# Optimization experiments

Measured on AMD Instinct MI355X. Metric: run time of the kernel, lower is better.

The kernel has to match this reference:

```python
import jax, jax.numpy as jnp
import numpy as np

B, H, W, C = 8, 128, 128, 192
G, K = 6, 3
K2 = K * K
GC = C // G
OFFSET_SCALE = 0.1
DN = ('NHWC', 'HWIO', 'NHWC')


def setup_inputs() -> dict:
    key = jax.random.key(0)
    ks = jax.random.split(key, 8)
    s = 1.0 / np.sqrt(C)
    return {
        'x': jax.random.normal(ks[0], (B, H, W, C), jnp.float32),
        'w_in': jax.random.normal(ks[1], (C, C), jnp.float32) * s,
        'b_in': jnp.zeros((C,), jnp.float32),
        'w_dw': jax.random.normal(ks[2], (3, 3, 1, C), jnp.float32) / 3.0,  # depthwise 3x3, HWIO
        'b_dw': jnp.zeros((C,), jnp.float32),
        'w_pw': jax.random.normal(ks[3], (1, 1, C, C), jnp.float32) * s,  # 1x1 conv
        'b_pw': jnp.zeros((C,), jnp.float32),
        'w_off': jax.random.normal(ks[4], (C, G * K2 * 2), jnp.float32) * 0.01,
        'b_off': jnp.zeros((G * K2 * 2,), jnp.float32),
        'w_mask': jax.random.normal(ks[5], (C, G * K2), jnp.float32) * 0.01,
        'b_mask': jnp.zeros((G * K2,), jnp.float32),
        'w_out': jax.random.normal(ks[6], (C, C), jnp.float32) * s,
        'b_out': jnp.zeros((C,), jnp.float32),
    }


def _deform_forward(x, w_in, b_in, w_dw, b_dw, w_pw, b_pw, w_off, b_off, w_mask, b_mask, w_out, b_out):
    x_proj = x @ w_in + b_in  # [B,H,W,C]

    # dw_conv: depthwise 3x3 -> SiLU -> 1x1 pointwise (all channels-last)
    xd = jax.lax.conv_general_dilated(x, w_dw, (1, 1), 'SAME', dimension_numbers=DN,
                                      feature_group_count=C) + b_dw
    xd = xd * jax.nn.sigmoid(xd)  # SiLU
    xd = jax.lax.conv_general_dilated(xd, w_pw, (1, 1), 'SAME', dimension_numbers=DN) + b_pw

    offsets = (xd @ w_off + b_off).reshape(B, H, W, G, K2, 2) * OFFSET_SCALE
    attn = jax.nn.softmax((xd @ w_mask + b_mask).reshape(B, H, W, G, K2), axis=-1)
    attn = jnp.nan_to_num(attn, nan=0.0)

    r = jnp.arange(-(K // 2), K // 2 + 1, dtype=jnp.float32)
    ref_grid = jnp.stack(jnp.meshgrid(r, r, indexing='ij'), -1).reshape(K2, 2)  # [K2,2]
    pos = ref_grid + offsets  # [B,H,W,G,K2,2]
    pos_h = jnp.clip(pos[..., 0] + jnp.arange(H, dtype=jnp.float32)[None, :, None, None, None], 0.0, H - 1)
    pos_w = jnp.clip(pos[..., 1] + jnp.arange(W, dtype=jnp.float32)[None, None, :, None, None], 0.0, W - 1)

    xg = x_proj.reshape(B, H * W, G, GC)

    def gather(hi, wi):
        idx = (hi * W + wi).reshape(B, H * W, G, 1)
        return jnp.take_along_axis(xg, idx, axis=1).reshape(B, H, W, G, GC)

    def tap(acc, inputs):
        ph, pw, a = inputs  # each [B,H,W,G]
        hf = jnp.clip(ph.astype(jnp.int32), 0, H - 1)
        wf = jnp.clip(pw.astype(jnp.int32), 0, W - 1)
        hc = jnp.minimum(hf + 1, H - 1)
        wc = jnp.minimum(wf + 1, W - 1)
        hw = ph - hf.astype(jnp.float32)
        ww = pw - wf.astype(jnp.float32)
        sampled = (gather(hf, wf) * ((1 - hw) * (1 - ww))[..., None]
                   + gather(hf, wc) * ((1 - hw) * ww)[..., None]
                   + gather(hc, wf) * (hw * (1 - ww))[..., None]
                   + gather(hc, wc) * (hw * ww)[..., None])
        return acc + sampled * a[..., None], None

    xs = (jnp.moveaxis(pos_h, -1, 0), jnp.moveaxis(pos_w, -1, 0), jnp.moveaxis(attn, -1, 0))
    out, _ = jax.lax.scan(tap, jnp.zeros((B, H, W, G, GC), x.dtype), xs)
    return out.reshape(B, H, W, C) @ w_out + b_out


def reference(x, w_in, b_in, w_dw, b_dw, w_pw, b_pw, w_off, b_off, w_mask, b_mask, w_out, b_out):
    return _deform_forward(x, w_in, b_in, w_dw, b_dw, w_pw, b_pw,
                           w_off, b_off, w_mask, b_mask, w_out, b_out)
```

## Files before the change

kernel.cpp:

```cpp
#include <hip/hip_runtime.h>
#include <hip/hip_bf16.h>

#define Bn 8
#define Hn 128
#define Wn 128
#define Cn 192
#define Gn 6
#define GCn 32
#define NPIX (Bn*Hn*Wn)

typedef __attribute__((ext_vector_type(8))) short v8s;
typedef __attribute__((ext_vector_type(4))) float v4f;
typedef __attribute__((ext_vector_type(2))) float v2f;
typedef __hip_bfloat16 bf16;

__device__ __forceinline__ float b2f(bf16 v){ return __bfloat162float(v); }
__device__ __forceinline__ float lo16(unsigned u){ return __uint_as_float(u << 16); }
__device__ __forceinline__ float hi16(unsigned u){ return __uint_as_float(u & 0xffff0000u); }
__device__ __forceinline__ v2f up2(unsigned u){
    return (v2f){ __uint_as_float(u << 16), __uint_as_float(u & 0xffff0000u) };
}

__global__ __launch_bounds__(256) void cvt_bf16(const float* __restrict__ in,
                                                bf16* __restrict__ out, long n)
{
    long base = ((long)blockIdx.x*256 + threadIdx.x)*8;
    if (base >= n) return;
    float v[8];
    *(float4*)(v)   = *(const float4*)(in + base);
    *(float4*)(v+4) = *(const float4*)(in + base + 4);
    bf16 o[8];
    #pragma unroll
    for (int j=0;j<8;j++) o[j] = __float2bfloat16(v[j]);
    *(uint4*)(out + base) = *(uint4*)o;
}

__global__ __launch_bounds__(256) void swizzle_w(const float* __restrict__ w,
                                                 bf16* __restrict__ out, int N)
{
    int idx = blockIdx.x*256 + threadIdx.x;
    int j = idx & 7, lane = (idx>>3)&63, ks = (idx>>9)%6, nt = idx/3072;
    int k = ks*32 + ((lane>>4)<<3) + j;
    int n = (nt<<4) + (lane&15);
    out[idx] = (n < N) ? __float2bfloat16(w[k*N + n]) : __float2bfloat16(0.0f);
}

__global__ __launch_bounds__(256) void swizzle_om(const float* __restrict__ woff,
        const float* __restrict__ wmask, const float* __restrict__ boff,
        const float* __restrict__ bmask, bf16* __restrict__ out, float* __restrict__ biascat)
{
    int idx = blockIdx.x*256 + threadIdx.x;
    if (idx < 192) {
        float bv = 0.0f;
        if (idx < 108) bv = boff[idx];
        else if (idx < 162) bv = bmask[idx-108];
        biascat[idx] = bv;
    }
    int j = idx & 7, lane = (idx>>3)&63, ks = (idx>>9)%6, nt = idx/3072;
    int k = ks*32 + ((lane>>4)<<3) + j;
    int n = (nt<<4) + (lane&15);
    float v = 0.0f;
    if (n < 108)      v = woff[k*108 + n];
    else if (n < 162) v = wmask[k*54 + (n-108)];
    out[idx] = __float2bfloat16(v);
}

__device__ __forceinline__ void store_out(bf16* p, float v){ *p = __float2bfloat16(v); }
__device__ __forceinline__ void store_out(float* p, float v){ *p = v; }

template<typename OutT>
__global__ __launch_bounds__(256, 2) void gemm6r(const bf16* __restrict__ A,
        const v8s* __restrict__ wfrag, const float* __restrict__ bias,
        OutT* __restrict__ Cmat, int Nreal, int Nstride)
{
    int tid = threadIdx.x;
    int wave = tid >> 6, lane = tid & 63;
    int q = lane >> 4, r = lane & 15;
    int n = blockIdx.x;
    int l = (n & 7) * 128 + (n >> 3);
    int yhalf = l & 1;
    int mt0 = l >> 1;
    const v8s* wsrc = wfrag + yhalf*(36*64) + lane;
    v8s breg[36];
    #pragma unroll
    for (int f=0; f<36; f++) breg[f] = wsrc[f*64];
    int col0 = yhalf*96;
    float bv[6];
    #pragma unroll
    for (int nt=0; nt<6; nt++) {
        int col = col0 + nt*16 + r;
        bv[nt] = (col < Nreal) ? bias[col] : 0.0f;
    }
    const int MT = NPIX/64;
    for (int mt = mt0; mt < MT; mt += 512) {
        const bf16* Ap = A + (size_t)(mt*64 + wave*16 + r)*Cn + q*8;
        v8s av[6];
        #pragma unroll
        for (int ks=0; ks<6; ks++) av[ks] = *(const v8s*)(Ap + ks*32);
        v4f acc[6];
        #pragma unroll
        for (int nt=0;nt<6;nt++) acc[nt] = (v4f){0.f,0.f,0.f,0.f};
        #pragma unroll
        for (int ks=0; ks<6; ks++)
            #pragma unroll
            for (int nt=0;nt<6;nt++)
                acc[nt] = __builtin_amdgcn_mfma_f32_16x16x32_bf16(
                              av[ks], breg[nt*6+ks], acc[nt], 0, 0, 0);
        int orow = mt*64 + wave*16 + q*4;
        #pragma unroll
        for (int nt=0;nt<6;nt++) {
            int col = col0 + nt*16 + r;
            if (col < Nreal) {
                #pragma unroll
                for (int i=0;i<4;i++)
                    store_out(&Cmat[(size_t)(orow+i)*Nstride + col], acc[nt][i] + bv[nt]);
            }
        }
    }
}

__global__ __launch_bounds__(256, 4) void dw_silu(const bf16* __restrict__ x,
        const bf16* __restrict__ wdwb, const float* __restrict__ bdw, bf16* __restrict__ out)
{
    int bid = blockIdx.x;
    int bsw = (bid & 7) * 768 + (bid >> 3);
    int idx = bsw*256 + threadIdx.x;
    int c16 = idx % 12; int pix = idx / 12;
    int b = pix >> 14; int hw = pix & 16383; int h = hw >> 7, w = hw & 127;
    int cb = c16*16;
    v2f acc2[8];
    #pragma unroll
    for (int j=0;j<8;j++) acc2[j] = (v2f){bdw[cb+2*j], bdw[cb+2*j+1]};
    #pragma unroll
    for (int dy=-1;dy<=1;dy++){
        int hh=h+dy; if ((unsigned)hh >= (unsigned)Hn) continue;
        #pragma unroll
        for (int dx=-1;dx<=1;dx++){
            int ww=w+dx; if ((unsigned)ww >= (unsigned)Wn) continue;
            const uint4* xp = (const uint4*)(x + ((size_t)((b<<14)+(hh<<7)+ww))*Cn + cb);
            const uint4* wp = (const uint4*)(wdwb + ((dy+1)*3+(dx+1))*Cn + cb);
            #pragma unroll
            for (int cs=0;cs<2;cs++){
                uint4 xu = xp[cs], wu = wp[cs];
                unsigned xa[4] = {xu.x,xu.y,xu.z,xu.w};
                unsigned wa[4] = {wu.x,wu.y,wu.z,wu.w};
                #pragma unroll
                for (int t=0;t<4;t++)
                    acc2[cs*4+t] += up2(xa[t]) * up2(wa[t]);
            }
        }
    }
    bf16 ov[16];
    #pragma unroll
    for (int j=0;j<8;j++){
        float v0 = acc2[j].x, v1 = acc2[j].y;
        ov[2*j]   = __float2bfloat16(v0 / (1.f + __expf(-v0)));
        ov[2*j+1] = __float2bfloat16(v1 / (1.f + __expf(-v1)));
    }
    uint4* op = (uint4*)(out + (size_t)pix*Cn + cb);
    op[0] = ((uint4*)ov)[0];
    op[1] = ((uint4*)ov)[1];
}


#define LOADTAP(K, S)                                                        \
  { float ph = (float)(h + (K)/3 - 1) + 0.1f*lo16(op[K]);                    \
    float pw = (float)(w + (K)%3 - 1) + 0.1f*hi16(op[K]);                    \
    ph = fminf(fmaxf(ph, 0.f), 127.f);                                       \
    pw = fminf(fmaxf(pw, 0.f), 127.f);                                       \
    int hf = (int)ph, wf = (int)pw;                                          \
    fh##S = ph - (float)hf; fw##S = pw - (float)wf;                          \
    int hc = min(hf+1,127), wc = min(wf+1,127);                              \
    const uint4* p00 = (const uint4*)(xb + ((hf<<7)+wf)*Cn);                 \
    const uint4* p01 = (const uint4*)(xb + ((hf<<7)+wc)*Cn);                 \
    const uint4* p10 = (const uint4*)(xb + ((hc<<7)+wf)*Cn);                 \
    const uint4* p11 = (const uint4*)(xb + ((hc<<7)+wc)*Cn);                 \
    S##00[0]=p00[0]; S##00[1]=p00[1]; S##01[0]=p01[0]; S##01[1]=p01[1];      \
    S##10[0]=p10[0]; S##10[1]=p10[1]; S##11[0]=p11[0]; S##11[1]=p11[1]; }

#define ACCTAP(K, S)                                                         \
  { float a = att[K];                                                        \
    float w00=(1.f-fh##S)*(1.f-fw##S)*a, w01=(1.f-fh##S)*fw##S*a,            \
          w10=fh##S*(1.f-fw##S)*a, w11=fh##S*fw##S*a;                        \
    _Pragma("unroll")                                                        \
    for (int cs=0;cs<2;cs++){                                                \
      unsigned u00[4]={S##00[cs].x,S##00[cs].y,S##00[cs].z,S##00[cs].w};     \
      unsigned u01[4]={S##01[cs].x,S##01[cs].y,S##01[cs].z,S##01[cs].w};     \
      unsigned u10[4]={S##10[cs].x,S##10[cs].y,S##10[cs].z,S##10[cs].w};     \
      unsigned u11[4]={S##11[cs].x,S##11[cs].y,S##11[cs].z,S##11[cs].w};     \
      _Pragma("unroll")                                                      \
      for (int t=0;t<4;t++)                                                  \
        acc2[cs*4+t] += up2(u00[t])*w00 + up2(u01[t])*w01                    \
                      + up2(u10[t])*w10 + up2(u11[t])*w11; } }

__global__ __launch_bounds__(256, 4) void deform_sample(const bf16* __restrict__ P,
        const bf16* __restrict__ OM, bf16* __restrict__ S)
{
    int bid = blockIdx.x;
    int bsw = (bid & 7) * 768 + (bid >> 3);
    int idx = bsw*256 + threadIdx.x;
    int half = idx & 1;
    int g = (idx >> 1) % 6;
    int pix = idx / 12;
    int b = pix >> 14; int hw = pix & 16383; int h = hw >> 7, w = hw & 127;
    const bf16* om = OM + (size_t)pix*162;
    const bf16* oml = om + 108 + g*9;
    const unsigned* ofp = (const unsigned*)(om + g*18);

    unsigned op[9];
    #pragma unroll
    for (int k=0;k<9;k++) op[k] = ofp[k];

    float att[9];
    float m = -1e30f;
    #pragma unroll
    for (int k=0;k<9;k++){ att[k] = b2f(oml[k]); m = fmaxf(m, att[k]); }
    float ssum = 0.f;
    #pragma unroll
    for (int k=0;k<9;k++){ att[k] = __expf(att[k]-m); ssum += att[k]; }
    float inv = 1.f/ssum;
    #pragma unroll
    for (int k=0;k<9;k++) att[k] *= inv;

    int chbase = g*GCn + half*16;
    const bf16* xb = P + ((((size_t)b) << 14))*Cn + chbase;

    v2f acc2[8];
    #pragma unroll
    for (int j=0;j<8;j++) acc2[j] = (v2f){0.f, 0.f};

    uint4 A00[2],A01[2],A10[2],A11[2]; float fhA,fwA;
    uint4 B00[2],B01[2],B10[2],B11[2]; float fhB,fwB;

    LOADTAP(0, A)
    LOADTAP(1, B)
    ACCTAP(0, A)  LOADTAP(2, A)
    ACCTAP(1, B)  LOADTAP(3, B)
    ACCTAP(2, A)  LOADTAP(4, A)
    ACCTAP(3, B)  LOADTAP(5, B)
    ACCTAP(4, A)  LOADTAP(6, A)
    ACCTAP(5, B)  LOADTAP(7, B)
    ACCTAP(6, A)  LOADTAP(8, A)
    ACCTAP(7, B)
    ACCTAP(8, A)

    bf16 ov[16];
    #pragma unroll
    for (int j=0;j<8;j++){
        ov[2*j]   = __float2bfloat16(acc2[j].x);
        ov[2*j+1] = __float2bfloat16(acc2[j].y);
    }
    uint4* sp = (uint4*)(S + (size_t)pix*Cn + chbase);
    sp[0] = ((uint4*)ov)[0];
    sp[1] = ((uint4*)ov)[1];
}

extern "C" void kernel_launch(void* const* d_in, const int* in_sizes, int n_in,
                              void* d_out, int out_size, void* d_ws, size_t ws_size,
                              hipStream_t stream)
{
    const float* x      = (const float*)d_in[0];
    const float* w_in   = (const float*)d_in[1];
    const float* b_in   = (const float*)d_in[2];
    const float* w_dw   = (const float*)d_in[3];
    const float* b_dw   = (const float*)d_in[4];
    const float* w_pw   = (const float*)d_in[5];
    const float* b_pw   = (const float*)d_in[6];
    const float* w_off  = (const float*)d_in[7];
    const float* b_off  = (const float*)d_in[8];
    const float* w_mask = (const float*)d_in[9];
    const float* b_mask = (const float*)d_in[10];
    const float* w_out  = (const float*)d_in[11];
    const float* b_out  = (const float*)d_in[12];
    float* out = (float*)d_out;

    char* ws = (char*)d_ws;
    size_t off = 0;
    auto carve = [&](size_t bytes)->char* {
        char* p = ws + off; off += (bytes + 255) & ~(size_t)255; return p; };
    bf16* XB  = (bf16*)carve((size_t)NPIX*Cn*2);
    bf16* P   = (bf16*)carve((size_t)NPIX*Cn*2);
    bf16* D   = (bf16*)carve((size_t)NPIX*Cn*2);
    bf16* OM  = (bf16*)carve((size_t)NPIX*162*2);
    bf16* wfI = (bf16*)carve(36864*2);
    bf16* wfP = (bf16*)carve(36864*2);
    bf16* wfO = (bf16*)carve(36864*2);
    bf16* wfM = (bf16*)carve(36864*2);
    float* bM = (float*)carve(192*4);
    bf16* WDW = (bf16*)carve(1728*2);

    dim3 blk(256);
    cvt_bf16<<<12288, blk, 0, stream>>>(x, XB, (long)NPIX*Cn);
    cvt_bf16<<<1,     blk, 0, stream>>>(w_dw, WDW, 1728);
    swizzle_w<<<144, blk, 0, stream>>>(w_in,  wfI, 192);
    swizzle_w<<<144, blk, 0, stream>>>(w_pw,  wfP, 192);
    swizzle_w<<<144, blk, 0, stream>>>(w_out, wfO, 192);
    swizzle_om<<<144, blk, 0, stream>>>(w_off, w_mask, b_off, b_mask, wfM, bM);

    gemm6r<bf16><<<1024, blk, 0, stream>>>(XB, (const v8s*)wfI, b_in, P, 192, 192);

    dw_silu<<<6144, blk, 0, stream>>>(XB, WDW, b_dw, D);

    bf16* X2 = XB;
    gemm6r<bf16><<<1024, blk, 0, stream>>>(D,  (const v8s*)wfP, b_pw, X2, 192, 192);
    gemm6r<bf16><<<1024, blk, 0, stream>>>(X2, (const v8s*)wfM, bM,  OM, 162, 162);

    deform_sample<<<6144, blk, 0, stream>>>(P, OM, D);

    gemm6r<float><<<1024, blk, 0, stream>>>(D, (const v8s*)wfO, b_out, out, 192, 192);
}
```

Before: 418.9 us.

## Fold pointwise conv weights into offset/mask projection to drop one GEMM

Because the 1x1 pointwise conv and the offset/mask projection are both linear, the two weight matrices are premultiplied (w_pw @ [w_off|w_mask]) on device, and the pw bias is folded into the combined bias. This removes a full NPIX x 192 x 192 GEMM and the intermediate X2 write and read. The combined weight is computed with a naive per-element loop of 192 MACs in the setup kernel, which adds a small cost. Rounding changes because the bf16 rounding of the intermediate is skipped.

```diff
diff --git a/kernel.cpp b/kernel.cpp
--- a/kernel.cpp
+++ b/kernel.cpp
@@ -45,24 +45,35 @@
     out[idx] = (n < N) ? __float2bfloat16(w[k*N + n]) : __float2bfloat16(0.0f);
 }
 
-__global__ __launch_bounds__(256) void swizzle_om(const float* __restrict__ woff,
-        const float* __restrict__ wmask, const float* __restrict__ boff,
+__global__ __launch_bounds__(256) void swizzle_omc(const float* __restrict__ wpw,
+        const float* __restrict__ woff, const float* __restrict__ wmask,
+        const float* __restrict__ bpw, const float* __restrict__ boff,
         const float* __restrict__ bmask, bf16* __restrict__ out, float* __restrict__ biascat)
 {
     int idx = blockIdx.x*256 + threadIdx.x;
+    int j = idx & 7, lane = (idx>>3)&63, ks = (idx>>9)%6, nt = idx/3072;
+    int k = ks*32 + ((lane>>4)<<3) + j;
+    int m = (nt<<4) + (lane&15);
+    float acc = 0.0f;
+    if (m < 162) {
+        const float* wrow = wpw + k*192;
+        for (int n=0; n<192; n++) {
+            float wc = (m < 108) ? woff[n*108 + m] : wmask[n*54 + (m-108)];
+            acc += wrow[n] * wc;
+        }
+    }
+    out[idx] = __float2bfloat16(acc);
     if (idx < 192) {
         float bv = 0.0f;
-        if (idx < 108) bv = boff[idx];
-        else if (idx < 162) bv = bmask[idx-108];
+        if (idx < 162) {
+            bv = (idx < 108) ? boff[idx] : bmask[idx-108];
+            for (int n=0; n<192; n++) {
+                float wc = (idx < 108) ? woff[n*108 + idx] : wmask[n*54 + (idx-108)];
+                bv += bpw[n] * wc;
+            }
+        }
         biascat[idx] = bv;
     }
-    int j = idx & 7, lane = (idx>>3)&63, ks = (idx>>9)%6, nt = idx/3072;
-    int k = ks*32 + ((lane>>4)<<3) + j;
-    int n = (nt<<4) + (lane&15);
-    float v = 0.0f;
-    if (n < 108)      v = woff[k*108 + n];
-    else if (n < 162) v = wmask[k*54 + (n-108)];
-    out[idx] = __float2bfloat16(v);
 }
 
 __device__ __forceinline__ void store_out(bf16* p, float v){ *p = __float2bfloat16(v); }
@@ -283,7 +294,6 @@
     bf16* D   = (bf16*)carve((size_t)NPIX*Cn*2);
     bf16* OM  = (bf16*)carve((size_t)NPIX*162*2);
     bf16* wfI = (bf16*)carve(36864*2);
-    bf16* wfP = (bf16*)carve(36864*2);
     bf16* wfO = (bf16*)carve(36864*2);
     bf16* wfM = (bf16*)carve(36864*2);
     float* bM = (float*)carve(192*4);
@@ -293,17 +303,14 @@
     cvt_bf16<<<12288, blk, 0, stream>>>(x, XB, (long)NPIX*Cn);
     cvt_bf16<<<1,     blk, 0, stream>>>(w_dw, WDW, 1728);
     swizzle_w<<<144, blk, 0, stream>>>(w_in,  wfI, 192);
-    swizzle_w<<<144, blk, 0, stream>>>(w_pw,  wfP, 192);
     swizzle_w<<<144, blk, 0, stream>>>(w_out, wfO, 192);
-    swizzle_om<<<144, blk, 0, stream>>>(w_off, w_mask, b_off, b_mask, wfM, bM);
+    swizzle_omc<<<144, blk, 0, stream>>>(w_pw, w_off, w_mask, b_pw, b_off, b_mask, wfM, bM);
 
     gemm6r<bf16><<<1024, blk, 0, stream>>>(XB, (const v8s*)wfI, b_in, P, 192, 192);
 
     dw_silu<<<6144, blk, 0, stream>>>(XB, WDW, b_dw, D);
 
-    bf16* X2 = XB;
-    gemm6r<bf16><<<1024, blk, 0, stream>>>(D,  (const v8s*)wfP, b_pw, X2, 192, 192);
-    gemm6r<bf16><<<1024, blk, 0, stream>>>(X2, (const v8s*)wfM, bM,  OM, 162, 162);
+    gemm6r<bf16><<<1024, blk, 0, stream>>>(D, (const v8s*)wfM, bM, OM, 162, 162);
 
     deform_sample<<<6144, blk, 0, stream>>>(P, OM, D);
 
```

Result: no change. 418.5 us (-0.1%).
